# Optimization experiments

Hardware: AMD Instinct MI355X
Metric: run time of the kernel (lower is better)

## Reference

```python
import jax, jax.numpy as jnp
import numpy as np

N = 100000   # nodes
E = 1600000  # edges
IN, H, OUT = 128, 128, 40
BN_EPS = 1e-5


def setup_inputs() -> dict:
    key = jax.random.key(0)
    ks = jax.random.split(key, 8)
    x = jax.random.normal(ks[0], (N, IN), jnp.float32)
    edge_src = jax.random.randint(ks[1], (E,), 0, N, jnp.int32)
    edge_dst = jax.random.randint(ks[2], (E,), 0, N, jnp.int32)

    def glorot(k, shape):
        lim = (6.0 / (shape[0] + shape[1])) ** 0.5
        return jax.random.uniform(k, shape, jnp.float32, -lim, lim)

    return {
        "x": x, "edge_src": edge_src, "edge_dst": edge_dst,
        "W1": glorot(ks[3], (IN, H)), "b1": jnp.zeros((H,), jnp.float32),
        "g1": jnp.ones((H,), jnp.float32), "bt1": jnp.zeros((H,), jnp.float32),
        "W2": glorot(ks[4], (H, H)), "b2": jnp.zeros((H,), jnp.float32),
        "g2": jnp.ones((H,), jnp.float32), "bt2": jnp.zeros((H,), jnp.float32),
        "Wr": glorot(ks[5], (H, OUT)), "br": jnp.zeros((OUT,), jnp.float32),
    }


def _gcn_conv(h_in, W, b, src, dst, dinv):
    # GCNConv: D^{-1/2}(A+I)D^{-1/2} X W + b  (symmetric norm w/ self-loops)
    h = h_in @ W                                   # [N,H]
    coef = dinv[src] * dinv[dst]                   # [E]
    agg = jax.ops.segment_sum(h[src] * coef[:, None], dst, num_segments=N)
    agg = agg + h * (dinv * dinv)[:, None]         # self-loop contribution
    return agg + b


def _bn_relu(h, gamma, beta):
    # BatchNorm1d in training mode (batch stats, biased variance) + ReLU
    mean = jnp.mean(h, axis=0)
    var = jnp.var(h, axis=0)
    y = (h - mean) * jax.lax.rsqrt(var + BN_EPS) * gamma + beta
    return jax.nn.relu(y)


def reference(x, edge_src, edge_dst, W1, b1, g1, bt1, W2, b2, g2, bt2, Wr, br):
    ones = jnp.ones((E,), jnp.float32)
    deg = jax.ops.segment_sum(ones, edge_dst, num_segments=N) + 1.0  # +1 self-loop
    dinv = jax.lax.rsqrt(deg)

    h = _gcn_conv(x, W1, b1, edge_src, edge_dst, dinv)
    h = _bn_relu(h, g1, bt1)
    h = _gcn_conv(h, W2, b2, edge_src, edge_dst, dinv)
    h = _bn_relu(h, g2, bt2)
    # dropout omitted (deterministic eval); readout linear
    return h @ Wr + br
```

## Files before the change

### kernel.cpp

```cpp
#include <hip/hip_runtime.h>
#include <hip/hip_bf16.h>
#include <hip/hip_fp16.h>

#define H_DIM 128
#define CAP 48

typedef _Float16 half8 __attribute__((ext_vector_type(8)));
typedef float floatx4 __attribute__((ext_vector_type(4)));

__device__ inline int imax(int a, int b) { return a > b ? a : b; }
__device__ inline int imin(int a, int b) { return a < b ? a : b; }

__global__ void fill_cols_kernel(int4* __restrict__ cols4, int n4, int padv,
                                 int4* __restrict__ zbase, int zn4,
                                 float2* __restrict__ zrowA, float2* __restrict__ zrowB) {
    int i = blockIdx.x * 256 + threadIdx.x;
    if (blockIdx.x == 0 && threadIdx.x < 32) {
        zrowA[threadIdx.x] = make_float2(0.f, 0.f);
        zrowB[threadIdx.x] = make_float2(0.f, 0.f);
    }
    if (i < zn4) {
        int4 zv; zv.x = 0; zv.y = 0; zv.z = 0; zv.w = 0;
        zbase[i] = zv;
    }
    if (i < n4) {
        int4 v; v.x = padv; v.y = padv; v.z = padv; v.w = padv;
        cols4[i] = v;
    }
}

__global__ void csr_fill_kernel(const int4* __restrict__ src4, const int4* __restrict__ dst4,
                                int* __restrict__ cursor, int* __restrict__ cols,
                                int E_, int N_, int shift) {
    int b = blockIdx.x & 7;
    if (((N_ - 1) >> shift) < b) return;
    int i4 = (blockIdx.x >> 3) * 256 + threadIdx.x;
    int base = i4 * 4;
    if (base >= E_) return;
    int4 d4 = dst4[i4];
    int4 s4 = src4[i4];
#pragma unroll
    for (int u = 0; u < 4; ++u) {
        int e = base + u;
        int d = (&d4.x)[u];
        if (e < E_ && (d >> shift) == b) {
            int p = d * CAP + atomicAdd(&cursor[d], 1);
            cols[p] = (&s4.x)[u] << 8;
        }
    }
}

__device__ inline half8 a_frag_f32(const float* Xr, int k0) {
    float4 v0 = *(const float4*)(Xr + k0);
    float4 v1 = *(const float4*)(Xr + k0 + 4);
    half8 a;
    a[0] = (_Float16)v0.x; a[1] = (_Float16)v0.y; a[2] = (_Float16)v0.z; a[3] = (_Float16)v0.w;
    a[4] = (_Float16)v1.x; a[5] = (_Float16)v1.y; a[6] = (_Float16)v1.z; a[7] = (_Float16)v1.w;
    return a;
}
__device__ inline half8 a_frag_f16_bn(const _Float16* Xr, int k0,
                                      const float* A, const float* B) {
    half8 r = *(const half8*)(Xr + k0);
    float4 a0 = *(const float4*)(A + k0);
    float4 a1 = *(const float4*)(A + k0 + 4);
    float4 b0 = *(const float4*)(B + k0);
    float4 b1 = *(const float4*)(B + k0 + 4);
    half8 o;
    o[0] = (_Float16)fmaxf(fmaf((float)r[0], a0.x, b0.x), 0.f);
    o[1] = (_Float16)fmaxf(fmaf((float)r[1], a0.y, b0.y), 0.f);
    o[2] = (_Float16)fmaxf(fmaf((float)r[2], a0.z, b0.z), 0.f);
    o[3] = (_Float16)fmaxf(fmaf((float)r[3], a0.w, b0.w), 0.f);
    o[4] = (_Float16)fmaxf(fmaf((float)r[4], a1.x, b1.x), 0.f);
    o[5] = (_Float16)fmaxf(fmaf((float)r[5], a1.y, b1.y), 0.f);
    o[6] = (_Float16)fmaxf(fmaf((float)r[6], a1.z, b1.z), 0.f);
    o[7] = (_Float16)fmaxf(fmaf((float)r[7], a1.w, b1.w), 0.f);
    return o;
}

template<bool BN, typename InT>
__global__ __launch_bounds__(256) void gemm_mfma_kernel(
    const InT* __restrict__ X, const float* __restrict__ W,
    const float* __restrict__ gsum, const float* __restrict__ gsq,
    const float* __restrict__ gamma, const float* __restrict__ beta,
    const int* __restrict__ cnt,
    _Float16* __restrict__ Y, int N_)
{
    __shared__ _Float16 Wf[32 * 64 * 8];
    __shared__ __align__(16) float Alds[128], Blds[128];

    const int tid = threadIdx.x;
    if constexpr (BN) {
        if (tid < 128) {
            float inv_n = 1.0f / (float)N_;
            float mean = gsum[tid] * inv_n;
            float var  = gsq[tid] * inv_n - mean * mean;
            float a = rsqrtf(var + 1e-5f) * gamma[tid];
            Alds[tid] = a;
            Blds[tid] = beta[tid] - mean * a;
        }
    }
    for (int idx = tid; idx < 128 * 32; idx += 256) {
        int k = idx >> 5;
        int n0 = (idx & 31) * 4;
        float4 w = *(const float4*)(W + k * 128 + n0);
        int kb = k >> 5, q = (k >> 3) & 3, j = k & 7;
#pragma unroll
        for (int u = 0; u < 4; ++u) {
            int n = n0 + u;
            int lane = (n & 15) | (q << 4);
            Wf[((((n >> 4) * 4 + kb) * 64 + lane) << 3) + j] = (_Float16)((&w.x)[u]);
        }
    }
    __syncthreads();

    const int wv = tid >> 6, lane = tid & 63;
    const int m = lane & 15, q = lane >> 4;
    const int row0 = blockIdx.x * 64 + wv * 16;

    int arow = row0 + m;
    if (arow >= N_) arow = N_ - 1;
    const InT* Xr = X + (size_t)arow * H_DIM;

    half8 a[4];
#pragma unroll
    for (int kb = 0; kb < 4; ++kb) {
        int k0 = kb * 32 + q * 8;
        if constexpr (BN) a[kb] = a_frag_f16_bn((const _Float16*)Xr, k0, Alds, Blds);
        else              a[kb] = a_frag_f32((const float*)Xr, k0);
    }

    floatx4 acc[8];
#pragma unroll
    for (int nt = 0; nt < 8; ++nt) acc[nt] = (floatx4){0.f, 0.f, 0.f, 0.f};

#pragma unroll
    for (int nt = 0; nt < 8; ++nt) {
#pragma unroll
        for (int kb = 0; kb < 4; ++kb) {
            half8 b = *(const half8*)&Wf[(((nt * 4 + kb) * 64 + lane) << 3)];
            acc[nt] = __builtin_amdgcn_mfma_f32_16x16x32_f16(a[kb], b, acc[nt], 0, 0, 0);
        }
    }

#pragma unroll
    for (int r = 0; r < 4; ++r) {
        int row = row0 + q * 4 + r;
        if (row < N_) {
            float ds = rsqrtf((float)cnt[row] + 1.0f);
            _Float16* Yr = Y + (size_t)row * H_DIM + m;
#pragma unroll
            for (int nt = 0; nt < 8; ++nt)
                Yr[nt * 16] = (_Float16)(ds * acc[nt][r]);
        }
    }
}

__global__ __launch_bounds__(256) void readout_mfma_kernel(
    const _Float16* __restrict__ X, const float* __restrict__ W,
    const float* __restrict__ gsum, const float* __restrict__ gsq,
    const float* __restrict__ gamma, const float* __restrict__ beta,
    const float* __restrict__ br,
    float* __restrict__ Y, int N_, int OUTC)
{
    __shared__ _Float16 Wf[12 * 64 * 8];
    __shared__ __align__(16) float Alds[128], Blds[128];

    const int tid = threadIdx.x;
    if (tid < 128) {
        float inv_n = 1.0f / (float)N_;
        float mean = gsum[tid] * inv_n;
        float var  = gsq[tid] * inv_n - mean * mean;
        float a = rsqrtf(var + 1e-5f) * gamma[tid];
        Alds[tid] = a;
        Blds[tid] = beta[tid] - mean * a;
    }
    for (int idx = tid; idx < 128 * 64; idx += 256) {
        int k = idx >> 6, n = idx & 63;
        if (n < 48) {
            float w = (n < OUTC) ? W[k * OUTC + n] : 0.f;
            int kb = k >> 5, q = (k >> 3) & 3, j = k & 7;
            int lane = (n & 15) | (q << 4);
            Wf[((((n >> 4) * 4 + kb) * 64 + lane) << 3) + j] = (_Float16)w;
        }
    }
    __syncthreads();

    const int wv = tid >> 6, lane = tid & 63;
    const int m = lane & 15, q = lane >> 4;
    const int row0 = blockIdx.x * 64 + wv * 16;

    int arow = row0 + m;
    if (arow >= N_) arow = N_ - 1;
    const _Float16* Xr = X + (size_t)arow * H_DIM;

    half8 a[4];
#pragma unroll
    for (int kb = 0; kb < 4; ++kb)
        a[kb] = a_frag_f16_bn(Xr, kb * 32 + q * 8, Alds, Blds);

    floatx4 acc[3];
#pragma unroll
    for (int nt = 0; nt < 3; ++nt) acc[nt] = (floatx4){0.f, 0.f, 0.f, 0.f};

#pragma unroll
    for (int nt = 0; nt < 3; ++nt) {
#pragma unroll
        for (int kb = 0; kb < 4; ++kb) {
            half8 b = *(const half8*)&Wf[(((nt * 4 + kb) * 64 + lane) << 3)];
            acc[nt] = __builtin_amdgcn_mfma_f32_16x16x32_f16(a[kb], b, acc[nt], 0, 0, 0);
        }
    }

#pragma unroll
    for (int nt = 0; nt < 3; ++nt) {
        int col = nt * 16 + m;
        if (col < OUTC) {
            float bb = br[col];
#pragma unroll
            for (int r = 0; r < 4; ++r) {
                int row = row0 + q * 4 + r;
                if (row < N_)
                    Y[(size_t)row * OUTC + col] = acc[nt][r] + bb;
            }
        }
    }
}

__global__ __launch_bounds__(256) void aggregate_stats_kernel(
    const __half2* __restrict__ Gp,
    const int* __restrict__ cnt,
    const int* __restrict__ cols,
    const float* __restrict__ bias,
    __half2* __restrict__ out,
    float* __restrict__ gsum, float* __restrict__ gsq,
    int N_, int stride)
{
    const int wave = threadIdx.x >> 6;
    const int lane = threadIdx.x & 63;
    const int c2 = lane * 2;
    const float bs0 = bias[c2], bs1 = bias[c2 + 1];
    const char* gpb = (const char*)Gp;
    const unsigned lane4 = (unsigned)lane * 4u;
    const __half2 z = __float2half2_rn(0.f);

    float r0 = 0.f, r1 = 0.f, q0 = 0.f, q1 = 0.f;

    const int n0 = blockIdx.x * 4 + wave;
    int dC = __builtin_amdgcn_readfirstlane(cnt[n0]);
    int n1 = n0 + stride; if (n1 > N_ - 1) n1 = N_ - 1;
    int dN = __builtin_amdgcn_readfirstlane(cnt[n1]);
    int c[24];
#pragma unroll
    for (int u = 0; u < 24; ++u) c[u] = cols[n0 * CAP + u];

    for (int n = n0; n < N_; n += stride) {
        __half2 self = *(const __half2*)(gpb + (((unsigned)n << 8) + lane4));
        __half2 h[24];
#pragma unroll
        for (int u = 0; u < 24; ++u)
            h[u] = *(const __half2*)(gpb + ((unsigned)c[u] + lane4));

        int n2 = n + 2 * stride; if (n2 > N_ - 1) n2 = N_ - 1;
        int dNN = __builtin_amdgcn_readfirstlane(cnt[n2]);

        int nn = n + stride; if (nn > N_ - 1) nn = N_ - 1;
        const int nb = nn * CAP;
#pragma unroll
        for (int u = 0; u < 24; ++u) c[u] = cols[nb + u];

        __half2 acc[8];
        acc[0] = self;
#pragma unroll
        for (int u = 1; u < 8; ++u) acc[u] = z;
#pragma unroll
        for (int u = 0; u < 24; ++u)
            acc[u & 7] = __hadd2(acc[u & 7], h[u]);

        int pd = (dC + 7) & ~7; if (pd < 24) pd = 24;
        const int e0 = n * CAP;
        for (int e = e0 + 24; e < e0 + pd; e += 8) {
            __half2 t[8];
#pragma unroll
            for (int u = 0; u < 8; ++u)
                t[u] = *(const __half2*)(gpb + ((unsigned)cols[e + u] + lane4));
#pragma unroll
            for (int u = 0; u < 8; ++u) acc[u] = __hadd2(acc[u], t[u]);
        }

        __half2 p0 = __hadd2(__hadd2(acc[0], acc[1]), __hadd2(acc[2], acc[3]));
        __half2 p1 = __hadd2(__hadd2(acc[4], acc[5]), __hadd2(acc[6], acc[7]));
        float2 F0 = __half22float2(p0);
        float2 F1 = __half22float2(p1);
        float di = rsqrtf((float)dC + 1.0f);
        float o0 = fmaf(di, F0.x + F1.x, bs0);
        float o1 = fmaf(di, F0.y + F1.y, bs1);
        out[((size_t)n << 6) + lane] = __floats2half2_rn(o0, o1);

        r0 += o0; r1 += o1;
        q0 = fmaf(o0, o0, q0); q1 = fmaf(o1, o1, q1);

        dC = dN; dN = dNN;
    }

    __shared__ float ssum[4][128], ssq[4][128];
    ssum[wave][c2] = r0; ssum[wave][c2 + 1] = r1;
    ssq[wave][c2]  = q0; ssq[wave][c2 + 1]  = q1;
    __syncthreads();
    if (threadIdx.x < 128) {
        int k = threadIdx.x;
        float s = (ssum[0][k] + ssum[1][k]) + (ssum[2][k] + ssum[3][k]);
        float q = (ssq[0][k] + ssq[1][k]) + (ssq[2][k] + ssq[3][k]);
        atomicAdd(&gsum[k], s);
        atomicAdd(&gsq[k], q);
    }
}

extern "C" void kernel_launch(void* const* d_in, const int* in_sizes, int n_in,
                              void* d_out, int out_size, void* d_ws, size_t ws_size,
                              hipStream_t stream) {
    const float* x   = (const float*)d_in[0];
    const int* esrc  = (const int*)d_in[1];
    const int* edst  = (const int*)d_in[2];
    const float* W1  = (const float*)d_in[3];
    const float* b1  = (const float*)d_in[4];
    const float* g1  = (const float*)d_in[5];
    const float* bt1 = (const float*)d_in[6];
    const float* W2  = (const float*)d_in[7];
    const float* b2  = (const float*)d_in[8];
    const float* g2  = (const float*)d_in[9];
    const float* bt2 = (const float*)d_in[10];
    const float* Wr  = (const float*)d_in[11];
    const float* br  = (const float*)d_in[12];

    const int N_ = in_sizes[0] / H_DIM;
    const int E_ = in_sizes[1];
    const int OUTC = out_size / N_;

    char* p = (char*)d_ws;
    auto alloc = [&](size_t bytes) -> void* {
        void* r = (void*)p;
        p += (bytes + 255) & ~(size_t)255;
        return r;
    };
    __half* tmpA = (__half*)alloc((size_t)(N_ + 1) * H_DIM * 2);
    __half* tmpB = (__half*)alloc((size_t)(N_ + 1) * H_DIM * 2);
    int*   cols  = (int*)  alloc(((size_t)N_ * CAP + 64) * 4);
    size_t cur_sz = ((size_t)N_ * 4 + 255) & ~(size_t)255;
    int*   cursor= (int*)  alloc((size_t)N_ * 4);
    float* bnbuf = (float*)alloc(8 * 128 * 4);
    float* sum1 = bnbuf,       *sq1 = bnbuf + 128;
    float* sum2 = bnbuf + 256, *sq2 = bnbuf + 384;

    const int eb4 = (E_ / 4 + 255) / 256;
    const int ntiles64 = (N_ + 63) / 64;
    const int n4 = N_ * CAP / 4;
    const int zn4 = (int)((cur_sz + 512 * 4) / 16);

    int shift = 0;
    while (((N_ - 1) >> shift) > 7) ++shift;

    const int AGG_BLOCKS = 2048;
    const int AGG_STRIDE = AGG_BLOCKS * 4;

    fill_cols_kernel<<<(n4 + 255) / 256, 256, 0, stream>>>(
        (int4*)cols, n4, N_ << 8, (int4*)cursor, zn4,
        (float2*)(tmpA + (size_t)N_ * H_DIM), (float2*)(tmpB + (size_t)N_ * H_DIM));
    csr_fill_kernel<<<eb4 * 8, 256, 0, stream>>>(
        (const int4*)esrc, (const int4*)edst, cursor, cols, E_, N_, shift);

    gemm_mfma_kernel<false, float><<<ntiles64, 256, 0, stream>>>(
        x, W1, nullptr, nullptr, nullptr, nullptr, cursor, (_Float16*)tmpA, N_);
    aggregate_stats_kernel<<<AGG_BLOCKS, 256, 0, stream>>>(
        (const __half2*)tmpA, cursor, cols, b1, (__half2*)tmpB,
        sum1, sq1, N_, AGG_STRIDE);

    gemm_mfma_kernel<true, _Float16><<<ntiles64, 256, 0, stream>>>(
        (const _Float16*)tmpB, W2, sum1, sq1, g1, bt1, cursor, (_Float16*)tmpA, N_);
    aggregate_stats_kernel<<<AGG_BLOCKS, 256, 0, stream>>>(
        (const __half2*)tmpA, cursor, cols, b2, (__half2*)tmpB,
        sum2, sq2, N_, AGG_STRIDE);

    readout_mfma_kernel<<<ntiles64, 256, 0, stream>>>(
        (const _Float16*)tmpB, Wr, sum2, sq2, g2, bt2, br, (float*)d_out, N_, OUTC);
}
```

Baseline: 436.0 us.

## Double-buffer neighbor gathers into LDS via async global_load_lds prefetch

The first 24 neighbor-row gathers of each node are issued for the next node one iteration ahead. They use global_load_lds DMA into a per-wave double-buffered shared-memory stage, replacing direct register loads. The aim is to hide gather latency by overlapping the next node's loads with the current node's accumulation. In exchange the kernel uses about 49KB of LDS per block, which may cut occupancy. Correctness relies on the compiler inserting the right wait before the staged data is read.

Result: slower. 464.1 us (+6.4%).

```diff
diff --git a/kernel.cpp b/kernel.cpp
--- a/kernel.cpp
+++ b/kernel.cpp
@@ -4,12 +4,20 @@
 
 #define H_DIM 128
 #define CAP 48
+#define KB  24
 
 typedef _Float16 half8 __attribute__((ext_vector_type(8)));
 typedef float floatx4 __attribute__((ext_vector_type(4)));
 
 __device__ inline int imax(int a, int b) { return a > b ? a : b; }
 __device__ inline int imin(int a, int b) { return a < b ? a : b; }
+#define RF(x) __builtin_amdgcn_readfirstlane(x)
+
+__device__ inline void gload_lds4(const void* g, void* l) {
+    __builtin_amdgcn_global_load_lds(
+        (const __attribute__((address_space(1))) void*)g,
+        (__attribute__((address_space(3))) void*)l, 4, 0, 0);
+}
 
 __global__ void fill_cols_kernel(int4* __restrict__ cols4, int n4, int padv,
                                  int4* __restrict__ zbase, int zn4,
@@ -235,6 +243,9 @@
     float* __restrict__ gsum, float* __restrict__ gsq,
     int N_, int stride)
 {
+    __shared__ __half2 stage[4][2][KB * 64];
+    __shared__ float ssum[4][128], ssq[4][128];
+
     const int wave = threadIdx.x >> 6;
     const int lane = threadIdx.x & 63;
     const int c2 = lane * 2;
@@ -245,40 +256,48 @@
 
     float r0 = 0.f, r1 = 0.f, q0 = 0.f, q1 = 0.f;
 
-    const int n0 = blockIdx.x * 4 + wave;
-    int dC = __builtin_amdgcn_readfirstlane(cnt[n0]);
-    int n1 = n0 + stride; if (n1 > N_ - 1) n1 = N_ - 1;
-    int dN = __builtin_amdgcn_readfirstlane(cnt[n1]);
-    int c[24];
-#pragma unroll
-    for (int u = 0; u < 24; ++u) c[u] = cols[n0 * CAP + u];
-
-    for (int n = n0; n < N_; n += stride) {
+    const int gw = blockIdx.x * 4 + wave;
+    int dC = RF(cnt[gw]);
+    int n1 = gw + stride; if (n1 > N_ - 1) n1 = N_ - 1;
+    int dN = RF(cnt[n1]);
+
+    int c[KB];
+#pragma unroll
+    for (int u = 0; u < KB; ++u) c[u] = cols[gw * CAP + u];
+#pragma unroll
+    for (int u = 0; u < KB; ++u)
+        gload_lds4(gpb + ((unsigned)c[u] + lane4), &stage[wave][0][u * 64]);
+#pragma unroll
+    for (int u = 0; u < KB; ++u) c[u] = cols[n1 * CAP + u];
+
+    int cur = 0;
+    for (int n = gw; n < N_; n += stride) {
         __half2 self = *(const __half2*)(gpb + (((unsigned)n << 8) + lane4));
-        __half2 h[24];
-#pragma unroll
-        for (int u = 0; u < 24; ++u)
-            h[u] = *(const __half2*)(gpb + ((unsigned)c[u] + lane4));
+
+        __half2* bufC = &stage[wave][0][0] + (size_t)cur * (KB * 64);
+        __half2* bufN = &stage[wave][0][0] + (size_t)(cur ^ 1) * (KB * 64);
+
+#pragma unroll
+        for (int u = 0; u < KB; ++u)
+            gload_lds4(gpb + ((unsigned)c[u] + lane4), bufN + u * 64);
 
         int n2 = n + 2 * stride; if (n2 > N_ - 1) n2 = N_ - 1;
-        int dNN = __builtin_amdgcn_readfirstlane(cnt[n2]);
-
-        int nn = n + stride; if (nn > N_ - 1) nn = N_ - 1;
-        const int nb = nn * CAP;
-#pragma unroll
-        for (int u = 0; u < 24; ++u) c[u] = cols[nb + u];
+        int dNN = RF(cnt[n2]);
+        const int nb = n2 * CAP;
+#pragma unroll
+        for (int u = 0; u < KB; ++u) c[u] = cols[nb + u];
 
         __half2 acc[8];
         acc[0] = self;
 #pragma unroll
         for (int u = 1; u < 8; ++u) acc[u] = z;
 #pragma unroll
-        for (int u = 0; u < 24; ++u)
-            acc[u & 7] = __hadd2(acc[u & 7], h[u]);
-
-        int pd = (dC + 7) & ~7; if (pd < 24) pd = 24;
+        for (int u = 0; u < KB; ++u)
+            acc[u & 7] = __hadd2(acc[u & 7], bufC[u * 64 + lane]);
+
+        int pd = (dC + 7) & ~7; if (pd < KB) pd = KB;
         const int e0 = n * CAP;
-        for (int e = e0 + 24; e < e0 + pd; e += 8) {
+        for (int e = e0 + KB; e < e0 + pd; e += 8) {
             __half2 t[8];
 #pragma unroll
             for (int u = 0; u < 8; ++u)
@@ -299,10 +318,9 @@
         r0 += o0; r1 += o1;
         q0 = fmaf(o0, o0, q0); q1 = fmaf(o1, o1, q1);
 
-        dC = dN; dN = dNN;
-    }
-
-    __shared__ float ssum[4][128], ssq[4][128];
+        dC = dN; dN = dNN; cur ^= 1;
+    }
+
     ssum[wave][c2] = r0; ssum[wave][c2 + 1] = r1;
     ssq[wave][c2]  = q0; ssq[wave][c2 + 1]  = q1;
     __syncthreads();
```
